# Optimization experiments

Hardware: AMD Instinct MI355X
Metric: run time of the kernel (lower is better)

Reference implementation:

```python
import jax, jax.numpy as jnp
import numpy as np

B, TC, TQ, D = 32, 2048, 256, 256

def setup_inputs() -> dict:
    key = jax.random.key(0)
    k1, k2, k3 = jax.random.split(key, 3)
    context_emb = jax.random.normal(k1, (B, TC, D), dtype=jnp.float32)
    query_emb = jax.random.normal(k2, (B, TQ, D), dtype=jnp.float32)
    # nn.Linear(3d, 1, bias=False) weight flattened to [3d]
    w = jax.random.normal(k3, (3 * D,), dtype=jnp.float32) * (1.0 / np.sqrt(3 * D))
    return {"context_emb": context_emb, "query_emb": query_emb, "w": w}

def reference(context_emb, query_emb, w):
    d = context_emb.shape[-1]
    w1, w2, w3 = w[:d], w[d:2*d], w[2*d:]
    # Trilinear similarity S[b,t,q] = c.w1 + q.w2 + (c*q).w3 -- equivalent to
    # Linear over cat(c_ext, q_ext, c_ext*q_ext) without materializing [B,Tc,Tq,3d].
    S = (jnp.einsum('btd,d->bt', context_emb, w1)[:, :, None]
         + jnp.einsum('bqd,d->bq', query_emb, w2)[:, None, :]
         + jnp.einsum('btd,bqd->btq', context_emb * w3, query_emb))  # [B,Tc,Tq]
    S_softmax_row = jax.nn.softmax(S, axis=2)              # [B,Tc,Tq]
    b_t = jax.nn.softmax(jnp.max(S, axis=2), axis=1)       # [B,Tc]
    U_attention = jnp.einsum('btq,bqd->btd', S_softmax_row, query_emb)  # [B,Tc,d]
    h = jnp.einsum('bt,btd->bd', b_t, context_emb)         # [B,d]
    H_attention = h[:, None, :]                            # broadcast over Tc
    G = jnp.concatenate(
        (context_emb,
         U_attention,
         context_emb * U_attention,
         context_emb * H_attention), axis=-1)              # [B,Tc,4d]
    return G
```

## Files before the change

### kernel.cpp

```cpp
#include <hip/hip_runtime.h>

#define NB  32
#define NTC 2048
#define NTQ 256
#define ND  256

#define HP2_OFF 0
#define H_OFF   266240
#define Q2_OFF  274432
#define QBF_OFF 282624
#define QT_OFF  (282624 + 1048576)

#define PSTR 264
#define USTR 130

typedef __attribute__((ext_vector_type(8))) short short8v;
typedef __attribute__((ext_vector_type(4))) float float4v;
typedef unsigned int u32;

static __device__ inline short f2bf(float f) {
  union { float f; unsigned u; } v; v.f = f;
  unsigned r = v.u + 0x7FFFu + ((v.u >> 16) & 1u);
  return (short)(r >> 16);
}

static __device__ inline void gload_lds16(const short* g, short* l) {
  __builtin_amdgcn_global_load_lds(
      (const __attribute__((address_space(1))) u32*)g,
      (__attribute__((address_space(3))) u32*)l, 16, 0, 0);
}

__global__ __launch_bounds__(256) void k0_prep(const float* __restrict__ qry,
                                               const float* __restrict__ w,
                                               float* __restrict__ q2_ws,
                                               short* __restrict__ Qbf,
                                               short* __restrict__ Qt) {
  __shared__ float sRed[8][32];
  const int tid = threadIdx.x;
  const int b = blockIdx.x >> 3;
  const int q0 = (blockIdx.x & 7) << 5;
  const int q = tid & 31;
  const int dc = tid >> 5;
  const float* src = qry + (((size_t)b * NTQ) + q0 + q) * ND + dc * 32;
  const float* w2p = w + ND + dc * 32;

  float vals[32];
  float part = 0.f;
  #pragma unroll
  for (int i = 0; i < 8; ++i) {
    float4 v = *(const float4*)(src + 4 * i);
    float4 u = *(const float4*)(w2p + 4 * i);
    part += v.x*u.x + v.y*u.y + v.z*u.z + v.w*u.w;
    vals[4*i] = v.x; vals[4*i+1] = v.y; vals[4*i+2] = v.z; vals[4*i+3] = v.w;
  }
  short pk[32];
  #pragma unroll
  for (int i = 0; i < 32; ++i) pk[i] = f2bf(vals[i]);

  short* dst = Qbf + ((size_t)b * NTQ + q0 + q) * ND + dc * 32;
  #pragma unroll
  for (int i = 0; i < 4; ++i) *(short8v*)(dst + 8 * i) = *(short8v*)(pk + 8 * i);
  short* dstT = Qt + (size_t)b * NTQ * ND + q0 + q;
  #pragma unroll
  for (int i = 0; i < 32; ++i) dstT[(size_t)(dc * 32 + i) * NTQ] = pk[i];

  part += __shfl_xor(part, 32);
  if ((tid & 32) == 0) sRed[dc][q] = part;
  __syncthreads();
  if (tid < 32) {
    float s = sRed[0][tid] + sRed[2][tid] + sRed[4][tid] + sRed[6][tid];
    q2_ws[b * NTQ + q0 + tid] = s;
  }
}

__global__ __launch_bounds__(256, 2) void k1_main(const float* __restrict__ ctx,
                                                  const float* __restrict__ w,
                                                  const short* __restrict__ Qbf,
                                                  const short* __restrict__ Qt,
                                                  const float* __restrict__ q2_ws,
                                                  float* __restrict__ hp2,
                                                  float* __restrict__ G) {
  __shared__ __align__(16) short sStage[2][256 * 32];
  __shared__ __align__(16) short sP_all[4 * 16 * PSTR];

  const int tid  = threadIdx.x;
  const int wv   = tid >> 6;
  const int lane = tid & 63;
  const int g    = lane >> 4;
  const int li   = lane & 15;
  const int bid  = blockIdx.x;
  const int obid = (bid & 7) * 128 + (bid >> 3);
  const int b    = obid >> 5;
  const int tile = obid & 31;
  const int t0   = tile << 6;

  short* sPw = sP_all + wv * (16 * PSTR);
  float* sUw = (float*)sPw;
  float* sH    = (float*)sStage;
  float* sMm   = (float*)sStage + 1024;
  float* sRedM = (float*)sStage + 1088;
  float* sRedZ = (float*)sStage + 1092;

  const float* __restrict__ ctxB = ctx + ((size_t)b * NTC + t0) * ND;
  const short* __restrict__ Qb   = Qbf + (size_t)b * NTQ * ND;
  const short* __restrict__ Qtb  = Qt  + (size_t)b * NTQ * ND;

  const int srow = 64 * wv + (lane >> 2);
  const int sblk = lane & 3;

  #define STAGE(buf, src, c0)                                                   \
    { _Pragma("unroll")                                                         \
      for (int j = 0; j < 4; ++j) {                                             \
        const int row_ = srow + 16 * j;                                         \
        const int gi_  = sblk ^ ((row_ >> 1) & 3);                              \
        gload_lds16((src) + (size_t)row_ * 256 + (c0) + 8 * gi_,                \
                    &sStage[buf][wv * 2048 + j * 512]);                         \
      } }

  float4v acc[16];
  #pragma unroll
  for (int n = 0; n < 16; ++n) acc[n] = (float4v)0.f;
  float s1part = 0.f;

  STAGE(0, Qb, 0);
  const float* arow = ctxB + (size_t)(16 * wv + li) * ND + 8 * g;
  float4 Ac0 = *(const float4*)(arow);
  float4 Ac1 = *(const float4*)(arow + 4);
  __syncthreads();

  for (int c = 0; c < 8; ++c) {
    float4 An0, An1;
    if (c < 7) {
      STAGE((c + 1) & 1, Qb, 32 * (c + 1));
      An0 = *(const float4*)(arow + 32 * (c + 1));
      An1 = *(const float4*)(arow + 32 * (c + 1) + 4);
    } else {
      STAGE(0, Qtb, 0);
    }
    const float* w1p = w + 32 * c + 8 * g;
    const float* w3p = w + 2 * ND + 32 * c + 8 * g;
    float4 u0 = *(const float4*)w1p, u1 = *(const float4*)(w1p + 4);
    float4 v0 = *(const float4*)w3p, v1 = *(const float4*)(w3p + 4);
    s1part += Ac0.x*u0.x + Ac0.y*u0.y + Ac0.z*u0.z + Ac0.w*u0.w
            + Ac1.x*u1.x + Ac1.y*u1.y + Ac1.z*u1.z + Ac1.w*u1.w;
    short8v af;
    af[0]=f2bf(Ac0.x*v0.x); af[1]=f2bf(Ac0.y*v0.y); af[2]=f2bf(Ac0.z*v0.z); af[3]=f2bf(Ac0.w*v0.w);
    af[4]=f2bf(Ac1.x*v1.x); af[5]=f2bf(Ac1.y*v1.y); af[6]=f2bf(Ac1.z*v1.z); af[7]=f2bf(Ac1.w*v1.w);
    const short* sb = sStage[c & 1];
    #pragma unroll
    for (int n = 0; n < 16; ++n) {
      const int row = 16 * n + li;
      short8v bb = *(const short8v*)(sb + row * 32 + 8 * (g ^ ((row >> 1) & 3)));
      acc[n] = __builtin_amdgcn_mfma_f32_16x16x32_bf16(af, bb, acc[n], 0, 0, 0);
    }
    __syncthreads();
    Ac0 = An0; Ac1 = An1;
  }

  s1part += __shfl_xor(s1part, 16);
  s1part += __shfl_xor(s1part, 32);
  float s1r[4];
  #pragma unroll
  for (int r = 0; r < 4; ++r) s1r[r] = __shfl(s1part, 4 * g + r);

  float q2v[16];
  #pragma unroll
  for (int n = 0; n < 16; ++n) q2v[n] = q2_ws[b * NTQ + 16 * n + li];

  #pragma unroll
  for (int n = 0; n < 16; ++n)
    #pragma unroll
    for (int r = 0; r < 4; ++r) acc[n][r] += s1r[r] + q2v[n];

  float mx[4], inv[4];
  #pragma unroll
  for (int r = 0; r < 4; ++r) {
    float m0 = acc[0][r];
    #pragma unroll
    for (int n = 1; n < 16; ++n) m0 = fmaxf(m0, acc[n][r]);
    m0 = fmaxf(m0, __shfl_xor(m0, 1));
    m0 = fmaxf(m0, __shfl_xor(m0, 2));
    m0 = fmaxf(m0, __shfl_xor(m0, 4));
    m0 = fmaxf(m0, __shfl_xor(m0, 8));
    mx[r] = m0;
  }
  #pragma unroll
  for (int r = 0; r < 4; ++r) {
    float z = 0.f;
    #pragma unroll
    for (int n = 0; n < 16; ++n) { float e = __expf(acc[n][r] - mx[r]); acc[n][r] = e; z += e; }
    z += __shfl_xor(z, 1);
    z += __shfl_xor(z, 2);
    z += __shfl_xor(z, 4);
    z += __shfl_xor(z, 8);
    inv[r] = 1.0f / z;
  }
  #pragma unroll
  for (int n = 0; n < 16; ++n) {
    #pragma unroll
    for (int r = 0; r < 4; ++r)
      sPw[(4 * g + r) * PSTR + 16 * n + li] = f2bf(acc[n][r] * inv[r]);
  }

  float4v acc2[16];
  #pragma unroll
  for (int n = 0; n < 16; ++n) acc2[n] = (float4v)0.f;

  for (int cc = 0; cc < 8; ++cc) {
    if (cc < 7) STAGE((cc + 1) & 1, Qtb, 32 * (cc + 1));
    const short* sb = sStage[cc & 1];
    short8v a2 = *(const short8v*)(sPw + li * PSTR + 32 * cc + 8 * g);
    #pragma unroll
    for (int n = 0; n < 16; ++n) {
      const int row = 16 * n + li;
      short8v bb = *(const short8v*)(sb + row * 32 + 8 * (g ^ ((row >> 1) & 3)));
      acc2[n] = __builtin_amdgcn_mfma_f32_16x16x32_bf16(a2, bb, acc2[n], 0, 0, 0);
    }
    if (cc < 7) __syncthreads();
  }

  if (li == 0) {
    #pragma unroll
    for (int r = 0; r < 4; ++r) sMm[16 * wv + 4 * g + r] = mx[r];
  }
  float lm = fmaxf(fmaxf(mx[0], mx[1]), fmaxf(mx[2], mx[3]));
  lm = fmaxf(lm, __shfl_xor(lm, 16));
  lm = fmaxf(lm, __shfl_xor(lm, 32));
  if (lane == 0) sRedM[wv] = lm;
  __syncthreads();
  const float Mloc = fmaxf(fmaxf(sRedM[0], sRedM[1]), fmaxf(sRedM[2], sRedM[3]));
  float zp = 0.f;
  #pragma unroll
  for (int r = 0; r < 4; ++r) zp += __expf(mx[r] - Mloc);
  zp += __shfl_xor(zp, 16);
  zp += __shfl_xor(zp, 32);
  if (lane == 0) sRedZ[wv] = zp;
  float wgt[4];
  #pragma unroll
  for (int k = 0; k < 4; ++k) wgt[k] = __expf(sMm[16 * wv + 4 * k + g] - Mloc);

  float4 ha[2][2];
  #pragma unroll
  for (int h = 0; h < 2; ++h)
    #pragma unroll
    for (int j = 0; j < 2; ++j) ha[h][j] = make_float4(0.f, 0.f, 0.f, 0.f);

  asm volatile("s_waitcnt lgkmcnt(0)" ::: "memory");
  __builtin_amdgcn_sched_barrier(0);
  #pragma unroll
  for (int h = 0; h < 2; ++h) {
    #pragma unroll
    for (int nn = 0; nn < 8; ++nn) {
      const int n = 8 * h + nn;
      #pragma unroll
      for (int r = 0; r < 4; ++r)
        sUw[(4 * g + r) * USTR + 16 * nn + li] = acc2[n][r];
    }
    asm volatile("s_waitcnt lgkmcnt(0)" ::: "memory");
    __builtin_amdgcn_sched_barrier(0);
    #pragma unroll
    for (int r0 = 0; r0 < 16; r0 += 4) {
      const int row = r0 + g;
      const float wk = wgt[r0 >> 2];
      #pragma unroll
      for (int j = 0; j < 2; ++j) {
        float4 u = *(const float4*)(sUw + row * USTR + 64 * j + 4 * li);
        const int gcol = 128 * h + 64 * j + 4 * li;
        const float* cp = ctxB + (size_t)(16 * wv + row) * ND + gcol;
        float4 c = *(const float4*)cp;
        const size_t gb = ((size_t)b * NTC + t0 + 16 * wv + row) * 1024 + gcol;
        *(float4*)(G + gb)       = c;
        *(float4*)(G + gb + 256) = u;
        *(float4*)(G + gb + 512) = make_float4(c.x*u.x, c.y*u.y, c.z*u.z, c.w*u.w);
        ha[h][j].x += wk * c.x; ha[h][j].y += wk * c.y;
        ha[h][j].z += wk * c.z; ha[h][j].w += wk * c.w;
      }
    }
    asm volatile("s_waitcnt lgkmcnt(0)" ::: "memory");
    __builtin_amdgcn_sched_barrier(0);
  }

  #pragma unroll
  for (int h = 0; h < 2; ++h)
    #pragma unroll
    for (int j = 0; j < 2; ++j) {
      float* f = (float*)&ha[h][j];
      #pragma unroll
      for (int e = 0; e < 4; ++e) {
        f[e] += __shfl_xor(f[e], 16);
        f[e] += __shfl_xor(f[e], 32);
      }
    }
  if (g == 0) {
    #pragma unroll
    for (int h = 0; h < 2; ++h)
      #pragma unroll
      for (int j = 0; j < 2; ++j)
        *(float4*)(sH + wv * 256 + 128 * h + 64 * j + 4 * li) = ha[h][j];
  }
  __syncthreads();
  float* hp = hp2 + (size_t)(b * 32 + tile) * 260;
  {
    float ph = sH[tid & 255] + sH[256 + (tid & 255)] + sH[512 + (tid & 255)] + sH[768 + (tid & 255)];
    if (tid < 256) hp[tid] = ph;
  }
  if (tid == 0) {
    hp[256] = Mloc;
    hp[257] = sRedZ[0] + sRedZ[1] + sRedZ[2] + sRedZ[3];
  }
}

__global__ __launch_bounds__(256) void k2h(const float* __restrict__ hp2,
                                           float* __restrict__ h_ws) {
  __shared__ float sM2[32], sZ2[32];
  const int b = blockIdx.x;
  const int tid = threadIdx.x;
  if (tid < 32) {
    sM2[tid] = hp2[(size_t)(b * 32 + tid) * 260 + 256];
    sZ2[tid] = hp2[(size_t)(b * 32 + tid) * 260 + 257];
  }
  __syncthreads();
  float M = -1e30f;
  #pragma unroll
  for (int i = 0; i < 32; ++i) M = fmaxf(M, sM2[i]);
  float Z = 0.f;
  float a = 0.f;
  #pragma unroll
  for (int i = 0; i < 32; ++i) {
    float e = __expf(sM2[i] - M);
    Z += sZ2[i] * e;
    a += hp2[(size_t)(b * 32 + i) * 260 + tid] * e;
  }
  h_ws[b * 256 + tid] = a / Z;
}

__global__ __launch_bounds__(256) void k3_epi(const float* __restrict__ ctx,
                                              const float* __restrict__ h_ws,
                                              float* __restrict__ G) {
  size_t f = (size_t)blockIdx.x * 256 + threadIdx.x;
  size_t e = f * 4;
  int d = (int)(e & 255);
  size_t bt = e >> 8;
  int b = (int)(bt >> 11);
  float4 c = *(const float4*)(ctx + e);
  float4 h = *(const float4*)(h_ws + b * ND + d);
  *(float4*)(G + bt * 1024 + 768 + d) =
      make_float4(c.x * h.x, c.y * h.y, c.z * h.z, c.w * h.w);
}

extern "C" void kernel_launch(void* const* d_in, const int* in_sizes, int n_in,
                              void* d_out, int out_size, void* d_ws, size_t ws_size,
                              hipStream_t stream) {
  const float* ctx = (const float*)d_in[0];
  const float* qry = (const float*)d_in[1];
  const float* w   = (const float*)d_in[2];
  float* G  = (float*)d_out;
  float* ws = (float*)d_ws;
  float* hp2   = ws + HP2_OFF;
  float* h_ws  = ws + H_OFF;
  float* q2_ws = ws + Q2_OFF;
  short* Qbf = (short*)(ws + QBF_OFF);
  short* Qt  = (short*)(ws + QT_OFF);

  k0_prep<<<NB * 8, 256, 0, stream>>>(qry, w, q2_ws, Qbf, Qt);
  k1_main<<<NB * (NTC / 64), 256, 0, stream>>>(ctx, w, Qbf, Qt, q2_ws, hp2, G);
  k2h<<<NB, 256, 0, stream>>>(hp2, h_ws);
  k3_epi<<<16384, 256, 0, stream>>>(ctx, h_ws, G);
}
```

Baseline: 115.9 us.

## Pipeline staging with explicit vmcnt barriers and write ctx slice of G during GEMM

Replaces __syncthreads in both MFMA loops with explicit s_waitcnt vmcnt counts plus s_barrier and sched_barrier fences. This lets the next chunk's async LDS staging stay in flight while the current chunk is computed. The w vector now goes into LDS once and q2 loads move earlier. The context copy into G is written from registers already loaded during the first GEMM instead of being reloaded in the epilogue. The hand-counted vmcnt values are fragile: the added G stores and early loads change how many memory ops are outstanding, which risks races or over-waiting.

```diff
diff --git a/kernel.cpp b/kernel.cpp
--- a/kernel.cpp
+++ b/kernel.cpp
@@ -82,6 +82,7 @@
                                                   float* __restrict__ G) {
   __shared__ __align__(16) short sStage[2][256 * 32];
   __shared__ __align__(16) short sP_all[4 * 16 * PSTR];
+  __shared__ __align__(16) float sW[768];
 
   const int tid  = threadIdx.x;
   const int wv   = tid >> 6;
@@ -122,30 +123,44 @@
   for (int n = 0; n < 16; ++n) acc[n] = (float4v)0.f;
   float s1part = 0.f;
 
+  float q2v[16];
+  #pragma unroll
+  for (int n = 0; n < 16; ++n) q2v[n] = q2_ws[b * NTQ + 16 * n + li];
+  if (tid < 192) *(float4*)(sW + 4 * tid) = *(const float4*)(w + 4 * tid);
   STAGE(0, Qb, 0);
   const float* arow = ctxB + (size_t)(16 * wv + li) * ND + 8 * g;
   float4 Ac0 = *(const float4*)(arow);
   float4 Ac1 = *(const float4*)(arow + 4);
-  __syncthreads();
-
+  asm volatile("s_waitcnt vmcnt(0) lgkmcnt(0)" ::: "memory");
+  __builtin_amdgcn_s_barrier();
+  __builtin_amdgcn_sched_barrier(0);
+
+  const size_t gb0 = ((size_t)b * NTC + t0 + 16 * wv + li) * 1024 + 8 * g;
+
+  #pragma unroll
   for (int c = 0; c < 8; ++c) {
-    float4 An0, An1;
-    if (c < 7) {
-      STAGE((c + 1) & 1, Qb, 32 * (c + 1));
-      An0 = *(const float4*)(arow + 32 * (c + 1));
-      An1 = *(const float4*)(arow + 32 * (c + 1) + 4);
-    } else {
-      STAGE(0, Qtb, 0);
-    }
-    const float* w1p = w + 32 * c + 8 * g;
-    const float* w3p = w + 2 * ND + 32 * c + 8 * g;
-    float4 u0 = *(const float4*)w1p, u1 = *(const float4*)(w1p + 4);
-    float4 v0 = *(const float4*)w3p, v1 = *(const float4*)(w3p + 4);
+    float4 u0 = *(const float4*)(sW + 32 * c + 8 * g);
+    float4 u1 = *(const float4*)(sW + 32 * c + 8 * g + 4);
+    float4 v0 = *(const float4*)(sW + 512 + 32 * c + 8 * g);
+    float4 v1 = *(const float4*)(sW + 512 + 32 * c + 8 * g + 4);
     s1part += Ac0.x*u0.x + Ac0.y*u0.y + Ac0.z*u0.z + Ac0.w*u0.w
             + Ac1.x*u1.x + Ac1.y*u1.y + Ac1.z*u1.z + Ac1.w*u1.w;
     short8v af;
     af[0]=f2bf(Ac0.x*v0.x); af[1]=f2bf(Ac0.y*v0.y); af[2]=f2bf(Ac0.z*v0.z); af[3]=f2bf(Ac0.w*v0.w);
     af[4]=f2bf(Ac1.x*v1.x); af[5]=f2bf(Ac1.y*v1.y); af[6]=f2bf(Ac1.z*v1.z); af[7]=f2bf(Ac1.w*v1.w);
+    __builtin_amdgcn_sched_barrier(0);
+    float4 An0, An1;
+    if (c < 7) {
+      An0 = *(const float4*)(arow + 32 * (c + 1));
+      An1 = *(const float4*)(arow + 32 * (c + 1) + 4);
+    }
+    __builtin_amdgcn_sched_barrier(0);
+    if (c < 7) { STAGE((c + 1) & 1, Qb, 32 * (c + 1)); }
+    else       { STAGE(0, Qtb, 0); }
+    __builtin_amdgcn_sched_barrier(0);
+    asm volatile("s_waitcnt vmcnt(6)" ::: "memory");
+    __builtin_amdgcn_s_barrier();
+    __builtin_amdgcn_sched_barrier(0);
     const short* sb = sStage[c & 1];
     #pragma unroll
     for (int n = 0; n < 16; ++n) {
@@ -153,7 +168,11 @@
       short8v bb = *(const short8v*)(sb + row * 32 + 8 * (g ^ ((row >> 1) & 3)));
       acc[n] = __builtin_amdgcn_mfma_f32_16x16x32_bf16(af, bb, acc[n], 0, 0, 0);
     }
-    __syncthreads();
+    *(float4*)(G + gb0 + 32 * c)     = Ac0;
+    *(float4*)(G + gb0 + 32 * c + 4) = Ac1;
+    __builtin_amdgcn_sched_barrier(0);
+    __builtin_amdgcn_s_barrier();
+    __builtin_amdgcn_sched_barrier(0);
     Ac0 = An0; Ac1 = An1;
   }
 
@@ -162,10 +181,6 @@
   float s1r[4];
   #pragma unroll
   for (int r = 0; r < 4; ++r) s1r[r] = __shfl(s1part, 4 * g + r);
-
-  float q2v[16];
-  #pragma unroll
-  for (int n = 0; n < 16; ++n) q2v[n] = q2_ws[b * NTQ + 16 * n + li];
 
   #pragma unroll
   for (int n = 0; n < 16; ++n)
@@ -206,17 +221,26 @@
   #pragma unroll
   for (int n = 0; n < 16; ++n) acc2[n] = (float4v)0.f;
 
+  #pragma unroll
   for (int cc = 0; cc < 8; ++cc) {
-    if (cc < 7) STAGE((cc + 1) & 1, Qtb, 32 * (cc + 1));
+    short8v a2 = *(const short8v*)(sPw + li * PSTR + 32 * cc + 8 * g);
+    __builtin_amdgcn_sched_barrier(0);
+    if (cc < 7) { STAGE((cc + 1) & 1, Qtb, 32 * (cc + 1)); }
+    __builtin_amdgcn_sched_barrier(0);
+    if (cc < 7) asm volatile("s_waitcnt vmcnt(4)" ::: "memory");
+    else        asm volatile("s_waitcnt vmcnt(0)" ::: "memory");
+    __builtin_amdgcn_s_barrier();
+    __builtin_amdgcn_sched_barrier(0);
     const short* sb = sStage[cc & 1];
-    short8v a2 = *(const short8v*)(sPw + li * PSTR + 32 * cc + 8 * g);
     #pragma unroll
     for (int n = 0; n < 16; ++n) {
       const int row = 16 * n + li;
       short8v bb = *(const short8v*)(sb + row * 32 + 8 * (g ^ ((row >> 1) & 3)));
       acc2[n] = __builtin_amdgcn_mfma_f32_16x16x32_bf16(a2, bb, acc2[n], 0, 0, 0);
     }
-    if (cc < 7) __syncthreads();
+    __builtin_amdgcn_sched_barrier(0);
+    __builtin_amdgcn_s_barrier();
+    __builtin_amdgcn_sched_barrier(0);
   }
 
   if (li == 0) {
@@ -269,7 +293,6 @@
         const float* cp = ctxB + (size_t)(16 * wv + row) * ND + gcol;
         float4 c = *(const float4*)cp;
         const size_t gb = ((size_t)b * NTC + t0 + 16 * wv + row) * 1024 + gcol;
-        *(float4*)(G + gb)       = c;
         *(float4*)(G + gb + 256) = u;
         *(float4*)(G + gb + 512) = make_float4(c.x*u.x, c.y*u.y, c.z*u.z, c.w*u.w);
         ha[h][j].x += wk * c.x; ha[h][j].y += wk * c.y;
@@ -308,6 +331,7 @@
     hp[256] = Mloc;
     hp[257] = sRedZ[0] + sRedZ[1] + sRedZ[2] + sRedZ[3];
   }
+  #undef STAGE
 }
 
 __global__ __launch_bounds__(256) void k2h(const float* __restrict__ hp2,
```

After: 108.2 us. 6.6% less time.
